# Optimization experiments

Hardware: AMD Instinct MI355X
Metric: run time of the kernel (lower is better)

Reference implementation:

```python
import jax, jax.numpy as jnp
import numpy as np

N = 100000
E = 1600000
D = 64    # input feat
H = 128   # hidden_channels
O = 64    # out_channels


def _sage(x, src, dst, Wl, bl, Wr, n_nodes):
    # mean-aggregate neighbor features: out[i] = mean_{(j->i)} x[j]
    msg = x[src]                                   # [E, F] gather
    agg = jax.ops.segment_sum(msg, dst, num_segments=n_nodes)
    cnt = jax.ops.segment_sum(jnp.ones((src.shape[0], 1), x.dtype), dst,
                              num_segments=n_nodes)
    mean = agg / jnp.maximum(cnt, 1.0)
    # SAGEConv: lin_l(aggr) + lin_r(x)  (bias lives in lin_l)
    return mean @ Wl + bl + x @ Wr


def setup_inputs() -> dict:
    key = jax.random.key(0)
    ks = jax.random.split(key, 12)
    s = lambda fan_in: 1.0 / np.sqrt(fan_in)
    x = jax.random.normal(ks[0], (N, D), dtype=jnp.float32)
    edge_index = jax.random.randint(ks[1], (2, E), 0, N, dtype=jnp.int64)
    return {
        "x": x,
        "edge_index": edge_index,
        "W1l": jax.random.uniform(ks[2], (D, H), jnp.float32, -s(D), s(D)),
        "b1": jax.random.uniform(ks[3], (H,), jnp.float32, -s(D), s(D)),
        "W1r": jax.random.uniform(ks[4], (D, H), jnp.float32, -s(D), s(D)),
        "Wlin1": jax.random.uniform(ks[5], (H, H), jnp.float32, -s(H), s(H)),
        "blin1": jax.random.uniform(ks[6], (H,), jnp.float32, -s(H), s(H)),
        "W2l": jax.random.uniform(ks[7], (H, H), jnp.float32, -s(H), s(H)),
        "b2": jax.random.uniform(ks[8], (H,), jnp.float32, -s(H), s(H)),
        "W2r": jax.random.uniform(ks[9], (H, H), jnp.float32, -s(H), s(H)),
        "Wlin2": jax.random.uniform(ks[10], (H, O), jnp.float32, -s(H), s(H)),
        "blin2": jax.random.uniform(ks[11], (O,), jnp.float32, -s(H), s(H)),
    }


def reference(x, edge_index, W1l, b1, W1r, Wlin1, blin1, W2l, b2, W2r, Wlin2, blin2):
    src, dst = edge_index[0], edge_index[1]
    h = jax.nn.relu(_sage(x, src, dst, W1l, b1, W1r, N))
    h = jax.nn.relu(h @ Wlin1 + blin1)
    h = jax.nn.relu(_sage(h, src, dst, W2l, b2, W2r, N))
    return h @ Wlin2 + blin2
```

## Files before the change

### kernel.cpp

```cpp
#include <hip/hip_runtime.h>
#include <cstddef>

static constexpr int NN = 100000;
static constexpr int NE = 1600000;
static constexpr int NODE_SHIFT = 8;
static constexpr int NB = (NN + 255) >> NODE_SHIFT;
static constexpr int CHUNK = 8192;
static constexpr int NCH = (NE + CHUNK - 1) / CHUNK;

typedef _Float16 f16x8 __attribute__((ext_vector_type(8)));
typedef float f32x4  __attribute__((ext_vector_type(4)));

__device__ __forceinline__ void acc8h(const uint4& v, float* a) {
    union { uint4 u; _Float16 h[8]; } t; t.u = v;
#pragma unroll
    for (int j = 0; j < 8; j++) a[j] += (float)t.h[j];
}


__global__ void zero_i32(int* p, int n) {
    int i = blockIdx.x * blockDim.x + threadIdx.x;
    if (i < n) p[i] = 0;
}

__global__ void bucket_count(const int* __restrict__ eidx, int* __restrict__ bcnt) {
    __shared__ int h[NB];
    for (int i = threadIdx.x; i < NB; i += 256) h[i] = 0;
    __syncthreads();
    int base = blockIdx.x * CHUNK;
    int end = min(base + CHUNK, NE);
    for (int e = base + threadIdx.x; e < end; e += 256)
        atomicAdd(&h[eidx[NE + e] >> NODE_SHIFT], 1);
    __syncthreads();
    for (int i = threadIdx.x; i < NB; i += 256)
        if (h[i]) atomicAdd(&bcnt[i], h[i]);
}

__global__ void bucket_scan(const int* __restrict__ bcnt, int* __restrict__ bbase,
                            int* __restrict__ bcur, int* __restrict__ row_ptr) {
    __shared__ int s[512];
    int t = threadIdx.x;
    int v = (t < NB) ? bcnt[t] : 0;
    s[t] = v; __syncthreads();
    for (int off = 1; off < 512; off <<= 1) {
        int x = (t >= off) ? s[t - off] : 0;
        __syncthreads();
        s[t] += x;
        __syncthreads();
    }
    if (t < NB) { int e = s[t] - v; bbase[t] = e; bcur[t] = e; }
    if (t == 0) { bbase[NB] = NE; row_ptr[NN] = NE; }
}

__global__ void bucket_scatter(const int* __restrict__ eidx, int* __restrict__ bcur,
                               uint2* __restrict__ pairs) {
    __shared__ int h[NB];
    __shared__ int cur[NB];
    __shared__ int off[NB];
    for (int i = threadIdx.x; i < NB; i += 256) { h[i] = 0; cur[i] = 0; }
    __syncthreads();
    int base = blockIdx.x * CHUNK;
    int end = min(base + CHUNK, NE);
    for (int e = base + threadIdx.x; e < end; e += 256)
        atomicAdd(&h[eidx[NE + e] >> NODE_SHIFT], 1);
    __syncthreads();
    for (int i = threadIdx.x; i < NB; i += 256)
        off[i] = h[i] ? atomicAdd(&bcur[i], h[i]) : 0;
    __syncthreads();
    for (int e = base + threadIdx.x; e < end; e += 256) {
        int d = eidx[NE + e], s = eidx[e];
        int b = d >> NODE_SHIFT;
        int p = atomicAdd(&cur[b], 1);
        pairs[off[b] + p] = make_uint2((unsigned)s, (unsigned)d);
    }
}

__launch_bounds__(256)
__global__ void bucket_csr(const uint2* __restrict__ pairs, const int* __restrict__ bbase,
                           int* __restrict__ row_ptr, int* __restrict__ ecsr) {
    __shared__ int hist[256];
    __shared__ int scn[256];
    __shared__ int cur[256];
    int b = blockIdx.x, t = threadIdx.x;
    int ebeg = bbase[b], eend = bbase[b + 1];
    int node0 = b << NODE_SHIFT;
    hist[t] = 0;
    __syncthreads();
    for (int e = ebeg + t; e < eend; e += 256)
        atomicAdd(&hist[pairs[e].y & 255u], 1);
    __syncthreads();
    int v = hist[t];
    scn[t] = v; __syncthreads();
    for (int off = 1; off < 256; off <<= 1) {
        int x = (t >= off) ? scn[t - off] : 0;
        __syncthreads();
        scn[t] += x;
        __syncthreads();
    }
    int excl = scn[t] - v;
    int node = node0 + t;
    if (node < NN) row_ptr[node] = ebeg + excl;
    cur[t] = excl;
    __syncthreads();
    for (int e = ebeg + t; e < eend; e += 256) {
        uint2 pr = pairs[e];
        int p = atomicAdd(&cur[pr.y & 255u], 1);
        ecsr[ebeg + p] = (int)pr.x;
    }
}


__global__ void convW(const float* __restrict__ W, unsigned short* __restrict__ Wt,
                      int K, int C, int wld, int kbase) {
    int t = blockIdx.x * blockDim.x + threadIdx.x;
    if (t >= K * C) return;
    int k = t / C, c = t % C;
    union { _Float16 h; unsigned short u; } cv;
    cv.h = (_Float16)W[t];
    Wt[(size_t)c * wld + kbase + k] = cv.u;
}

__global__ void convX(const float* __restrict__ x, unsigned short* __restrict__ bufP) {
    int t = blockIdx.x * blockDim.x + threadIdx.x;
    if (t >= NN * 64) return;
    int r = t >> 6, c = t & 63;
    union { _Float16 h; unsigned short u; } cv;
    cv.h = (_Float16)x[t];
    bufP[(size_t)r * 128 + 64 + c] = cv.u;
}


__launch_bounds__(256)
__global__ void agg1(const unsigned short* __restrict__ xp, const int* __restrict__ row_ptr,
                     const int* __restrict__ ecsr, unsigned short* __restrict__ outp) {
    constexpr int TPN = 8;
    int node = blockIdx.x * (256 / TPN) + threadIdx.x / TPN;
    int lane = threadIdx.x % TPN;
    if (node >= NN) return;
    int beg = row_ptr[node], end = row_ptr[node + 1];

    float a0[8] = {0,0,0,0,0,0,0,0}, a1[8] = {0,0,0,0,0,0,0,0};
    float a2[8] = {0,0,0,0,0,0,0,0}, a3[8] = {0,0,0,0,0,0,0,0};
    int i = beg;
    for (; i + 4 <= end; i += 4) {
        int s0 = ecsr[i], s1 = ecsr[i + 1], s2 = ecsr[i + 2], s3 = ecsr[i + 3];
        uint4 v0 = *(const uint4*)&xp[(size_t)s0 * 128 + 64 + lane * 8];
        uint4 v1 = *(const uint4*)&xp[(size_t)s1 * 128 + 64 + lane * 8];
        uint4 v2 = *(const uint4*)&xp[(size_t)s2 * 128 + 64 + lane * 8];
        uint4 v3 = *(const uint4*)&xp[(size_t)s3 * 128 + 64 + lane * 8];
        acc8h(v0, a0); acc8h(v1, a1); acc8h(v2, a2); acc8h(v3, a3);
    }
    for (; i < end; i++) {
        uint4 v0 = *(const uint4*)&xp[(size_t)ecsr[i] * 128 + 64 + lane * 8];
        acc8h(v0, a0);
    }
    int deg = end - beg;
    float r = (deg > 0) ? 1.f / (float)deg : 0.f;
    union { uint4 u; _Float16 h[8]; } o;
#pragma unroll
    for (int j = 0; j < 8; j++)
        o.h[j] = (_Float16)((a0[j] + a1[j] + a2[j] + a3[j]) * r);
    *(uint4*)(outp + (size_t)node * 128 + lane * 8) = o.u;
}

__launch_bounds__(256)
__global__ void agg2(const unsigned short* __restrict__ hbuf, const int* __restrict__ row_ptr,
                     const int* __restrict__ ecsr, unsigned short* __restrict__ outp) {
    constexpr int TPN = 16;
    int node = blockIdx.x * (256 / TPN) + threadIdx.x / TPN;
    int lane = threadIdx.x % TPN;
    if (node >= NN) return;
    int beg = row_ptr[node], end = row_ptr[node + 1];

    float a0[8] = {0,0,0,0,0,0,0,0}, a1[8] = {0,0,0,0,0,0,0,0};
    float a2[8] = {0,0,0,0,0,0,0,0}, a3[8] = {0,0,0,0,0,0,0,0};
    int i = beg;
    for (; i + 4 <= end; i += 4) {
        int s0 = ecsr[i], s1 = ecsr[i + 1], s2 = ecsr[i + 2], s3 = ecsr[i + 3];
        uint4 v0 = *(const uint4*)&hbuf[(size_t)s0 * 256 + 128 + lane * 8];
        uint4 v1 = *(const uint4*)&hbuf[(size_t)s1 * 256 + 128 + lane * 8];
        uint4 v2 = *(const uint4*)&hbuf[(size_t)s2 * 256 + 128 + lane * 8];
        uint4 v3 = *(const uint4*)&hbuf[(size_t)s3 * 256 + 128 + lane * 8];
        acc8h(v0, a0); acc8h(v1, a1); acc8h(v2, a2); acc8h(v3, a3);
    }
    for (; i < end; i++) {
        uint4 v0 = *(const uint4*)&hbuf[(size_t)ecsr[i] * 256 + 128 + lane * 8];
        acc8h(v0, a0);
    }
    int deg = end - beg;
    float r = (deg > 0) ? 1.f / (float)deg : 0.f;
    union { uint4 u; _Float16 h[8]; } o;
#pragma unroll
    for (int j = 0; j < 8; j++)
        o.h[j] = (_Float16)((a0[j] + a1[j] + a2[j] + a3[j]) * r);
    *(uint4*)(outp + (size_t)node * 256 + lane * 8) = o.u;
}

template<int K, int C, bool RELU, bool F16OUT>
__launch_bounds__(256, 4)
__global__ void gemm_f16(const unsigned short* __restrict__ A, int lda,
                         const unsigned short* __restrict__ Wt,
                         const float* __restrict__ bias,
                         unsigned short* __restrict__ outp, int old_, int obase,
                         float* __restrict__ outf) {
    constexpr int BM  = 128;
    constexpr int NKC = K / 64;
    constexpr int RT  = (C == 128) ? 4 : 2;
    __shared__ unsigned short As[BM * 72];
    __shared__ unsigned short Ws[C * 72];

    const int tid  = threadIdx.x;
    const int lane = tid & 63, wave = tid >> 6;
    const int lrow = lane & 15, quad = lane >> 4;
    const int wrow0 = (C == 128) ? (wave >> 1) * 64 : wave * 32;
    const int wcol0 = (C == 128) ? (wave & 1) * 64 : 0;
    const int row0  = blockIdx.x * BM;

    f32x4 acc[RT][4];
#pragma unroll
    for (int a = 0; a < RT; a++)
#pragma unroll
        for (int b = 0; b < 4; b++) acc[a][b] = (f32x4){0.f, 0.f, 0.f, 0.f};

#pragma unroll 1
    for (int it = 0; it < NKC; ++it) {
        int base = it * 64;
        for (int t = tid; t < BM * 8; t += 256) {
            int r = t >> 3, c8 = (t & 7) * 8;
            int gr = row0 + r;
            uint4 v = make_uint4(0u, 0u, 0u, 0u);
            if (gr < NN) v = *(const uint4*)&A[(size_t)gr * lda + base + c8];
            *(uint4*)&As[r * 72 + c8] = v;
        }
        for (int t = tid; t < C * 8; t += 256) {
            int wr = t >> 3, c8 = (t & 7) * 8;
            *(uint4*)&Ws[wr * 72 + c8] = *(const uint4*)&Wt[(size_t)wr * K + base + c8];
        }
        __syncthreads();
#pragma unroll
        for (int ks = 0; ks < 2; ++ks) {
            f16x8 af[RT], bfr[4];
#pragma unroll
            for (int rt = 0; rt < RT; rt++)
                af[rt] = *(const f16x8*)&As[(wrow0 + rt * 16 + lrow) * 72 + ks * 32 + quad * 8];
#pragma unroll
            for (int ct = 0; ct < 4; ct++)
                bfr[ct] = *(const f16x8*)&Ws[(wcol0 + ct * 16 + lrow) * 72 + ks * 32 + quad * 8];
#pragma unroll
            for (int rt = 0; rt < RT; rt++)
#pragma unroll
                for (int ct = 0; ct < 4; ct++)
                    acc[rt][ct] = __builtin_amdgcn_mfma_f32_16x16x32_f16(
                        af[rt], bfr[ct], acc[rt][ct], 0, 0, 0);
        }
        __syncthreads();
    }

    float bcol[4];
#pragma unroll
    for (int ct = 0; ct < 4; ct++) bcol[ct] = bias[wcol0 + ct * 16 + lrow];
#pragma unroll
    for (int rt = 0; rt < RT; rt++) {
#pragma unroll
        for (int ct = 0; ct < 4; ct++) {
#pragma unroll
            for (int r = 0; r < 4; r++) {
                int grow = row0 + wrow0 + rt * 16 + quad * 4 + r;
                if (grow < NN) {
                    int col = wcol0 + ct * 16 + lrow;
                    float v = acc[rt][ct][r] + bcol[ct];
                    if (RELU) v = fmaxf(v, 0.f);
                    if (F16OUT) {
                        union { _Float16 h; unsigned short u; } cv;
                        cv.h = (_Float16)v;
                        outp[(size_t)grow * old_ + obase + col] = cv.u;
                    } else {
                        outf[(size_t)grow * C + col] = v;
                    }
                }
            }
        }
    }
}


extern "C" void kernel_launch(void* const* d_in, const int* in_sizes, int n_in,
                              void* d_out, int out_size, void* d_ws, size_t ws_size,
                              hipStream_t stream) {
    const float* x     = (const float*)d_in[0];
    const int*   eidx  = (const int*)d_in[1];
    const float* W1l   = (const float*)d_in[2];
    const float* b1    = (const float*)d_in[3];
    const float* W1r   = (const float*)d_in[4];
    const float* Wlin1 = (const float*)d_in[5];
    const float* blin1 = (const float*)d_in[6];
    const float* W2l   = (const float*)d_in[7];
    const float* b2    = (const float*)d_in[8];
    const float* W2r   = (const float*)d_in[9];
    const float* Wlin2 = (const float*)d_in[10];
    const float* blin2 = (const float*)d_in[11];
    float* out = (float*)d_out;
    (void)in_sizes; (void)n_in; (void)out_size; (void)ws_size;

    char* ws = (char*)d_ws;
    size_t off = 0;
    auto alloc = [&](size_t bytes) -> void* {
        void* p = ws + off;
        off = (off + bytes + 255) & ~(size_t)255;
        return p;
    };
    int* bcnt    = (int*)alloc((size_t)NB * 4);
    int* bbase   = (int*)alloc((size_t)(NB + 1) * 4);
    int* bcur    = (int*)alloc((size_t)NB * 4);
    int* row_ptr = (int*)alloc((size_t)(NN + 1) * 4);
    int* ecsr    = (int*)alloc((size_t)NE * 4);
    uint2* pairs = (uint2*)alloc((size_t)NE * 8);
    unsigned short* Wt1  = (unsigned short*)alloc((size_t)128 * 128 * 2);
    unsigned short* Wtl1 = (unsigned short*)alloc((size_t)128 * 128 * 2);
    unsigned short* Wt2  = (unsigned short*)alloc((size_t)128 * 256 * 2);
    unsigned short* Wtf  = (unsigned short*)alloc((size_t)64  * 128 * 2);
    unsigned short* bufP = (unsigned short*)alloc((size_t)NN * 128 * 2);
    unsigned short* bufQ = (unsigned short*)alloc((size_t)NN * 256 * 2);
    unsigned short* bufR = (unsigned short*)alloc((size_t)NN * 128 * 2);

    zero_i32<<<(NB + 255) / 256, 256, 0, stream>>>(bcnt, NB);
    bucket_count<<<NCH, 256, 0, stream>>>(eidx, bcnt);
    bucket_scan<<<1, 512, 0, stream>>>(bcnt, bbase, bcur, row_ptr);
    bucket_scatter<<<NCH, 256, 0, stream>>>(eidx, bcur, pairs);
    bucket_csr<<<NB, 256, 0, stream>>>(pairs, bbase, row_ptr, ecsr);

    convW<<<32, 256, 0, stream>>>(W1l,   Wt1,  64, 128, 128, 0);
    convW<<<32, 256, 0, stream>>>(W1r,   Wt1,  64, 128, 128, 64);
    convW<<<64, 256, 0, stream>>>(Wlin1, Wtl1, 128, 128, 128, 0);
    convW<<<64, 256, 0, stream>>>(W2l,   Wt2,  128, 128, 256, 0);
    convW<<<64, 256, 0, stream>>>(W2r,   Wt2,  128, 128, 256, 128);
    convW<<<32, 256, 0, stream>>>(Wlin2, Wtf,  128, 64, 128, 0);

    convX<<<(NN * 64 + 255) / 256, 256, 0, stream>>>(x, bufP);
    agg1<<<(NN + 31) / 32, 256, 0, stream>>>(bufP, row_ptr, ecsr, bufP);

    const int GB128 = (NN + 127) / 128;

    gemm_f16<128, 128, true, true><<<GB128, 256, 0, stream>>>(
        bufP, 128, Wt1, b1, bufR, 128, 0, nullptr);
    gemm_f16<128, 128, true, true><<<GB128, 256, 0, stream>>>(
        bufR, 128, Wtl1, blin1, bufQ, 256, 128, nullptr);
    agg2<<<(NN + 15) / 16, 256, 0, stream>>>(bufQ, row_ptr, ecsr, bufQ);
    gemm_f16<256, 128, true, true><<<GB128, 256, 0, stream>>>(
        bufQ, 256, Wt2, b2, bufR, 128, 0, nullptr);
    gemm_f16<128, 64, false, false><<<GB128, 256, 0, stream>>>(
        bufR, 128, Wtf, blin2, nullptr, 0, 0, out);
}
```

Measured before the change: 333.5 us.

## Fuse conversion launches, unroll aggregation gathers, and register-prefetch GEMM tiles

Merges the zeroing, six weight-conversion and x-conversion kernels into one launch, cutting seven launches. The aggregation loops now issue eight independent gathers per iteration to raise memory-level parallelism. The GEMM prefetches the next K tile into registers while computing the current one, and its launch-bounds occupancy hint drops from 4 to 3 to make room for the extra registers. These are several unrelated changes, and the lower occupancy hint could offset the prefetch gain.

New measurement: 361.5 us. 8.4% more time.

```diff
diff --git a/kernel.cpp b/kernel.cpp
--- a/kernel.cpp
+++ b/kernel.cpp
@@ -17,11 +17,6 @@
     for (int j = 0; j < 8; j++) a[j] += (float)t.h[j];
 }
 
-
-__global__ void zero_i32(int* p, int n) {
-    int i = blockIdx.x * blockDim.x + threadIdx.x;
-    if (i < n) p[i] = 0;
-}
 
 __global__ void bucket_count(const int* __restrict__ eidx, int* __restrict__ bcnt) {
     __shared__ int h[NB];
@@ -109,24 +104,39 @@
     }
 }
 
-
-__global__ void convW(const float* __restrict__ W, unsigned short* __restrict__ Wt,
-                      int K, int C, int wld, int kbase) {
-    int t = blockIdx.x * blockDim.x + threadIdx.x;
-    if (t >= K * C) return;
-    int k = t / C, c = t % C;
+__global__ void conv_fused(const float* __restrict__ x,
+                           const float* __restrict__ W1l, const float* __restrict__ W1r,
+                           const float* __restrict__ Wlin1, const float* __restrict__ W2l,
+                           const float* __restrict__ W2r, const float* __restrict__ Wlin2,
+                           unsigned short* __restrict__ bufP, unsigned short* __restrict__ Wt1,
+                           unsigned short* __restrict__ Wtl1, unsigned short* __restrict__ Wt2,
+                           unsigned short* __restrict__ Wtf, int* __restrict__ bcnt) {
+    int bid = blockIdx.x, t = threadIdx.x;
     union { _Float16 h; unsigned short u; } cv;
-    cv.h = (_Float16)W[t];
-    Wt[(size_t)c * wld + kbase + k] = cv.u;
-}
-
-__global__ void convX(const float* __restrict__ x, unsigned short* __restrict__ bufP) {
-    int t = blockIdx.x * blockDim.x + threadIdx.x;
-    if (t >= NN * 64) return;
-    int r = t >> 6, c = t & 63;
-    union { _Float16 h; unsigned short u; } cv;
-    cv.h = (_Float16)x[t];
-    bufP[(size_t)r * 128 + 64 + c] = cv.u;
+    if (bid < 25000) {
+        int idx = bid * 256 + t;
+        int r = idx >> 6, c = idx & 63;
+        cv.h = (_Float16)x[idx];
+        bufP[(size_t)r * 128 + 64 + c] = cv.u;
+    } else if (bid >= 25288) {
+        int i = (bid - 25288) * 256 + t;
+        if (i < NB) bcnt[i] = 0;
+    } else {
+        int b = bid - 25000;
+        const float* W; unsigned short* Wt; int K, C, wld, kbase, base;
+        if (b < 32)       { W = W1l;   Wt = Wt1;  K = 64;  C = 128; wld = 128; kbase = 0;   base = b; }
+        else if (b < 64)  { W = W1r;   Wt = Wt1;  K = 64;  C = 128; wld = 128; kbase = 64;  base = b - 32; }
+        else if (b < 128) { W = Wlin1; Wt = Wtl1; K = 128; C = 128; wld = 128; kbase = 0;   base = b - 64; }
+        else if (b < 192) { W = W2l;   Wt = Wt2;  K = 128; C = 128; wld = 256; kbase = 0;   base = b - 128; }
+        else if (b < 256) { W = W2r;   Wt = Wt2;  K = 128; C = 128; wld = 256; kbase = 128; base = b - 192; }
+        else              { W = Wlin2; Wt = Wtf;  K = 128; C = 64;  wld = 128; kbase = 0;   base = b - 256; }
+        int idx = base * 256 + t;
+        if (idx < K * C) {
+            int k = idx / C, c = idx % C;
+            cv.h = (_Float16)W[idx];
+            Wt[(size_t)c * wld + kbase + k] = cv.u;
+        }
+    }
 }
 
 
@@ -142,8 +152,22 @@
     float a0[8] = {0,0,0,0,0,0,0,0}, a1[8] = {0,0,0,0,0,0,0,0};
     float a2[8] = {0,0,0,0,0,0,0,0}, a3[8] = {0,0,0,0,0,0,0,0};
     int i = beg;
+    for (; i + 8 <= end; i += 8) {
+        int s0 = ecsr[i], s1 = ecsr[i+1], s2 = ecsr[i+2], s3 = ecsr[i+3];
+        int s4 = ecsr[i+4], s5 = ecsr[i+5], s6 = ecsr[i+6], s7 = ecsr[i+7];
+        uint4 v0 = *(const uint4*)&xp[(size_t)s0 * 128 + 64 + lane * 8];
+        uint4 v1 = *(const uint4*)&xp[(size_t)s1 * 128 + 64 + lane * 8];
+        uint4 v2 = *(const uint4*)&xp[(size_t)s2 * 128 + 64 + lane * 8];
+        uint4 v3 = *(const uint4*)&xp[(size_t)s3 * 128 + 64 + lane * 8];
+        uint4 v4 = *(const uint4*)&xp[(size_t)s4 * 128 + 64 + lane * 8];
+        uint4 v5 = *(const uint4*)&xp[(size_t)s5 * 128 + 64 + lane * 8];
+        uint4 v6 = *(const uint4*)&xp[(size_t)s6 * 128 + 64 + lane * 8];
+        uint4 v7 = *(const uint4*)&xp[(size_t)s7 * 128 + 64 + lane * 8];
+        acc8h(v0, a0); acc8h(v1, a1); acc8h(v2, a2); acc8h(v3, a3);
+        acc8h(v4, a0); acc8h(v5, a1); acc8h(v6, a2); acc8h(v7, a3);
+    }
     for (; i + 4 <= end; i += 4) {
-        int s0 = ecsr[i], s1 = ecsr[i + 1], s2 = ecsr[i + 2], s3 = ecsr[i + 3];
+        int s0 = ecsr[i], s1 = ecsr[i+1], s2 = ecsr[i+2], s3 = ecsr[i+3];
         uint4 v0 = *(const uint4*)&xp[(size_t)s0 * 128 + 64 + lane * 8];
         uint4 v1 = *(const uint4*)&xp[(size_t)s1 * 128 + 64 + lane * 8];
         uint4 v2 = *(const uint4*)&xp[(size_t)s2 * 128 + 64 + lane * 8];
@@ -175,8 +199,22 @@
     float a0[8] = {0,0,0,0,0,0,0,0}, a1[8] = {0,0,0,0,0,0,0,0};
     float a2[8] = {0,0,0,0,0,0,0,0}, a3[8] = {0,0,0,0,0,0,0,0};
     int i = beg;
+    for (; i + 8 <= end; i += 8) {
+        int s0 = ecsr[i], s1 = ecsr[i+1], s2 = ecsr[i+2], s3 = ecsr[i+3];
+        int s4 = ecsr[i+4], s5 = ecsr[i+5], s6 = ecsr[i+6], s7 = ecsr[i+7];
+        uint4 v0 = *(const uint4*)&hbuf[(size_t)s0 * 256 + 128 + lane * 8];
+        uint4 v1 = *(const uint4*)&hbuf[(size_t)s1 * 256 + 128 + lane * 8];
+        uint4 v2 = *(const uint4*)&hbuf[(size_t)s2 * 256 + 128 + lane * 8];
+        uint4 v3 = *(const uint4*)&hbuf[(size_t)s3 * 256 + 128 + lane * 8];
+        uint4 v4 = *(const uint4*)&hbuf[(size_t)s4 * 256 + 128 + lane * 8];
+        uint4 v5 = *(const uint4*)&hbuf[(size_t)s5 * 256 + 128 + lane * 8];
+        uint4 v6 = *(const uint4*)&hbuf[(size_t)s6 * 256 + 128 + lane * 8];
+        uint4 v7 = *(const uint4*)&hbuf[(size_t)s7 * 256 + 128 + lane * 8];
+        acc8h(v0, a0); acc8h(v1, a1); acc8h(v2, a2); acc8h(v3, a3);
+        acc8h(v4, a0); acc8h(v5, a1); acc8h(v6, a2); acc8h(v7, a3);
+    }
     for (; i + 4 <= end; i += 4) {
-        int s0 = ecsr[i], s1 = ecsr[i + 1], s2 = ecsr[i + 2], s3 = ecsr[i + 3];
+        int s0 = ecsr[i], s1 = ecsr[i+1], s2 = ecsr[i+2], s3 = ecsr[i+3];
         uint4 v0 = *(const uint4*)&hbuf[(size_t)s0 * 256 + 128 + lane * 8];
         uint4 v1 = *(const uint4*)&hbuf[(size_t)s1 * 256 + 128 + lane * 8];
         uint4 v2 = *(const uint4*)&hbuf[(size_t)s2 * 256 + 128 + lane * 8];
@@ -197,7 +235,7 @@
 }
 
 template<int K, int C, bool RELU, bool F16OUT>
-__launch_bounds__(256, 4)
+__launch_bounds__(256, 3)
 __global__ void gemm_f16(const unsigned short* __restrict__ A, int lda,
                          const unsigned short* __restrict__ Wt,
                          const float* __restrict__ bias,
@@ -206,6 +244,8 @@
     constexpr int BM  = 128;
     constexpr int NKC = K / 64;
     constexpr int RT  = (C == 128) ? 4 : 2;
+    constexpr int NA  = BM * 8 / 256;
+    constexpr int NW  = C * 8 / 256;
     __shared__ unsigned short As[BM * 72];
     __shared__ unsigned short Ws[C * 72];
 
@@ -216,27 +256,45 @@
     const int wcol0 = (C == 128) ? (wave & 1) * 64 : 0;
     const int row0  = blockIdx.x * BM;
 
+    uint4 pa[NA], pw[NW];
+    auto loadA = [&](int it) {
+#pragma unroll
+        for (int j = 0; j < NA; j++) {
+            int tt = tid + j * 256; int r = tt >> 3, c8 = (tt & 7) * 8;
+            int gr = row0 + r;
+            pa[j] = (gr < NN) ? *(const uint4*)&A[(size_t)gr * lda + it * 64 + c8]
+                              : make_uint4(0u, 0u, 0u, 0u);
+        }
+    };
+    auto loadW = [&](int it) {
+#pragma unroll
+        for (int j = 0; j < NW; j++) {
+            int tt = tid + j * 256; int wr = tt >> 3, c8 = (tt & 7) * 8;
+            pw[j] = *(const uint4*)&Wt[(size_t)wr * K + it * 64 + c8];
+        }
+    };
+
     f32x4 acc[RT][4];
 #pragma unroll
     for (int a = 0; a < RT; a++)
 #pragma unroll
         for (int b = 0; b < 4; b++) acc[a][b] = (f32x4){0.f, 0.f, 0.f, 0.f};
 
+    loadA(0); loadW(0);
 #pragma unroll 1
     for (int it = 0; it < NKC; ++it) {
-        int base = it * 64;
-        for (int t = tid; t < BM * 8; t += 256) {
-            int r = t >> 3, c8 = (t & 7) * 8;
-            int gr = row0 + r;
-            uint4 v = make_uint4(0u, 0u, 0u, 0u);
-            if (gr < NN) v = *(const uint4*)&A[(size_t)gr * lda + base + c8];
-            *(uint4*)&As[r * 72 + c8] = v;
-        }
-        for (int t = tid; t < C * 8; t += 256) {
-            int wr = t >> 3, c8 = (t & 7) * 8;
-            *(uint4*)&Ws[wr * 72 + c8] = *(const uint4*)&Wt[(size_t)wr * K + base + c8];
-        }
-        __syncthreads();
+#pragma unroll
+        for (int j = 0; j < NA; j++) {
+            int tt = tid + j * 256; int r = tt >> 3, c8 = (tt & 7) * 8;
+            *(uint4*)&As[r * 72 + c8] = pa[j];
+        }
+#pragma unroll
+        for (int j = 0; j < NW; j++) {
+            int tt = tid + j * 256; int wr = tt >> 3, c8 = (tt & 7) * 8;
+            *(uint4*)&Ws[wr * 72 + c8] = pw[j];
+        }
+        __syncthreads();
+        if (it + 1 < NKC) { loadA(it + 1); loadW(it + 1); }
 #pragma unroll
         for (int ks = 0; ks < 2; ++ks) {
             f16x8 af[RT], bfr[4];
@@ -323,20 +381,14 @@
     unsigned short* bufQ = (unsigned short*)alloc((size_t)NN * 256 * 2);
     unsigned short* bufR = (unsigned short*)alloc((size_t)NN * 128 * 2);
 
-    zero_i32<<<(NB + 255) / 256, 256, 0, stream>>>(bcnt, NB);
+    conv_fused<<<25290, 256, 0, stream>>>(x, W1l, W1r, Wlin1, W2l, W2r, Wlin2,
+                                          bufP, Wt1, Wtl1, Wt2, Wtf, bcnt);
+
     bucket_count<<<NCH, 256, 0, stream>>>(eidx, bcnt);
     bucket_scan<<<1, 512, 0, stream>>>(bcnt, bbase, bcur, row_ptr);
     bucket_scatter<<<NCH, 256, 0, stream>>>(eidx, bcur, pairs);
     bucket_csr<<<NB, 256, 0, stream>>>(pairs, bbase, row_ptr, ecsr);
 
-    convW<<<32, 256, 0, stream>>>(W1l,   Wt1,  64, 128, 128, 0);
-    convW<<<32, 256, 0, stream>>>(W1r,   Wt1,  64, 128, 128, 64);
-    convW<<<64, 256, 0, stream>>>(Wlin1, Wtl1, 128, 128, 128, 0);
-    convW<<<64, 256, 0, stream>>>(W2l,   Wt2,  128, 128, 256, 0);
-    convW<<<64, 256, 0, stream>>>(W2r,   Wt2,  128, 128, 256, 128);
-    convW<<<32, 256, 0, stream>>>(Wlin2, Wtf,  128, 64, 128, 0);
-
-    convX<<<(NN * 64 + 255) / 256, 256, 0, stream>>>(x, bufP);
     agg1<<<(NN + 31) / 32, 256, 0, stream>>>(bufP, row_ptr, ecsr, bufP);
 
     const int GB128 = (NN + 127) / 128;
```
